# Optimization experiments

Hardware: AMD Instinct MI355X
Metric: run time of the kernel (lower is better)

The kernel has to match this reference:

```python
import jax, jax.numpy as jnp
import numpy as np

# ---- static config (matches init_kwargs) ----
NLAT, NLON = 181, 360
LMAX = NLAT                 # hard_thresholding_fraction = 1.0
MMAX = NLON // 2 + 1        # 181, real FFT in longitude
INC = 26
OUTC = 26
EMBED = 256
NLAYERS = 4
MLP_HID = int(EMBED * 2.0)
EPS = 1e-6


def _legendre(lmax, mmax, theta):
    """Orthonormal associated Legendre functions Pbar[l, m, k] at colatitudes theta."""
    ct, st = np.cos(theta), np.sin(theta)
    K = theta.size
    P = np.zeros((lmax, mmax, K), dtype=np.float64)
    P[0, 0] = np.sqrt(1.0 / (4.0 * np.pi))
    for m in range(1, mmax):
        P[m, m] = -np.sqrt((2.0 * m + 1.0) / (2.0 * m)) * st * P[m - 1, m - 1]
    for m in range(mmax):
        if m + 1 < lmax:
            P[m + 1, m] = np.sqrt(2.0 * m + 3.0) * ct * P[m, m]
        for l in range(m + 2, lmax):
            a = np.sqrt((4.0 * l * l - 1.0) / (l * l - m * m))
            b = np.sqrt(((2.0 * l + 1.0) * (l - 1.0 + m) * (l - 1.0 - m)) / ((2.0 * l - 3.0) * (l * l - m * m)))
            P[l, m] = a * ct * P[l - 1, m] - b * P[l - 2, m]
    return P

# equiangular grid + quadrature weights; precompute analysis/synthesis matrices
_theta = np.linspace(0.0, np.pi, NLAT)
_wq = (np.pi / (NLAT - 1)) * np.sin(_theta)
_P = _legendre(LMAX, MMAX, _theta)
PW = jnp.asarray((_P * (2.0 * np.pi * _wq)[None, None, :]).astype(np.float32))  # analysis
PS = jnp.asarray(_P.astype(np.float32))                                         # synthesis


def _ln(x):
    # per-pixel layer norm over channel dim, no affine (affine_norms=False)
    mu = jnp.mean(x, axis=1, keepdims=True)
    var = jnp.mean((x - mu) ** 2, axis=1, keepdims=True)
    return (x - mu) * jax.lax.rsqrt(var + EPS)


def _conv1x1(x, w, b=None):
    y = jnp.einsum('oi,bihw->bohw', w, x)
    return y if b is None else y + b[None, :, None, None]


def _sht(x):
    # x: (b,c,nlat,nlon) -> coeff (b,c,l,m) complex64
    F = jnp.fft.rfft(x, axis=-1) / NLON          # (b,c,k,m)
    return jnp.einsum('lmk,bckm->bclm', PW, F)


def _isht(c):
    F = jnp.einsum('lmk,bclm->bckm', PS, c)      # (b,c,k,m)
    return jnp.fft.irfft(F * NLON, n=NLON, axis=-1)


def _block(x, wsp, bsp, wis, bis, wf1, bf1, wf2, bf2):
    xn = _ln(x)                                  # norm0
    c = _sht(xn)
    co = jnp.einsum('oil,bilm->bolm', wsp, c)    # dhconv: diagonal in m, dense per l
    y = _isht(co) + bsp[None, :, None, None]
    x1 = y + _conv1x1(xn, wis, bis)              # inner linear skip (residual = filter input)
    x1 = jax.nn.gelu(x1, approximate=False)
    x2 = _ln(x1)                                 # norm1
    h = jax.nn.gelu(_conv1x1(x2, wf1, bf1), approximate=False)
    x2 = _conv1x1(h, wf2, bf2)                   # MLP
    return x2 + xn                               # outer identity skip


def setup_inputs() -> dict:
    key = jax.random.key(0)
    ks = jax.random.split(key, 10)
    n = jax.random.normal
    x = n(ks[0], (1, INC, NLAT, NLON), jnp.float32)
    w_enc = n(ks[1], (EMBED, INC), jnp.float32) * float(1.0 / np.sqrt(INC))
    b_enc = jnp.zeros((EMBED,), jnp.float32)
    pos_emb = n(ks[2], (1, EMBED, NLAT, NLON), jnp.float32) * 0.02
    w_spec = n(ks[3], (NLAYERS, EMBED, EMBED, LMAX), jnp.float32) * float(1.0 / np.sqrt(EMBED))
    b_spec = jnp.zeros((NLAYERS, EMBED), jnp.float32)
    w_iskip = n(ks[4], (NLAYERS, EMBED, EMBED), jnp.float32) * float(1.0 / np.sqrt(EMBED))
    b_iskip = jnp.zeros((NLAYERS, EMBED), jnp.float32)
    w_fc1 = n(ks[5], (NLAYERS, MLP_HID, EMBED), jnp.float32) * float(1.0 / np.sqrt(EMBED))
    b_fc1 = jnp.zeros((NLAYERS, MLP_HID), jnp.float32)
    w_fc2 = n(ks[6], (NLAYERS, EMBED, MLP_HID), jnp.float32) * float(1.0 / np.sqrt(MLP_HID))
    b_fc2 = jnp.zeros((NLAYERS, EMBED), jnp.float32)
    w_dec = n(ks[7], (OUTC, EMBED + INC), jnp.float32) * float(1.0 / np.sqrt(EMBED + INC))
    b_dec = jnp.zeros((OUTC,), jnp.float32)
    return {'x': x, 'w_enc': w_enc, 'b_enc': b_enc, 'pos_emb': pos_emb,
            'w_spec': w_spec, 'b_spec': b_spec, 'w_iskip': w_iskip, 'b_iskip': b_iskip,
            'w_fc1': w_fc1, 'b_fc1': b_fc1, 'w_fc2': w_fc2, 'b_fc2': b_fc2,
            'w_dec': w_dec, 'b_dec': b_dec}


def reference(x, w_enc, b_enc, pos_emb, w_spec, b_spec, w_iskip, b_iskip,
              w_fc1, b_fc1, w_fc2, b_fc2, w_dec, b_dec):
    res = x                                       # big_skip residual (raw input)
    h = _conv1x1(x, w_enc, b_enc) + pos_emb       # encoder + pos embed
    for i in range(NLAYERS):
        h = _block(h, w_spec[i], b_spec[i], w_iskip[i], b_iskip[i],
                   w_fc1[i], b_fc1[i], w_fc2[i], b_fc2[i])
    h = jnp.concatenate([h, res], axis=1)         # big skip concat
    return _conv1x1(h, w_dec, b_dec)
```

## Files before the change

### kernel.cpp

```cpp
#include <hip/hip_runtime.h>
#include <math.h>

#define NLATg 181
#define NLONg 360
#define PIXg  65160
#define EMBg  256
#define MHIDg 512
#define PLANEg 8386816
#define PKSTR 184
#define PMSTR2 33304

#define FLAG_GELU 1
#define FLAG_ACC  2
#define FLAG_F32  4
#define FLAG_BF16 8

typedef unsigned short u16;
typedef unsigned int   u32;
typedef __attribute__((ext_vector_type(8))) short bf16x8;
typedef __attribute__((ext_vector_type(4))) float f32x4;

__device__ __forceinline__ float gelu_f(float x) {
    return 0.5f * x * (1.0f + erff(x * 0.70710678118654752440f));
}

__device__ __forceinline__ void split_f(float v, u16& h, u16& l) {
    u32 u = __float_as_uint(v);
    h = (u16)(u >> 16);
    float hf = __uint_as_float(u & 0xFFFF0000u);
    l = (u16)(__float_as_uint(v - hf) >> 16);
}

__device__ __forceinline__ void glds16(const u16* g, u16* l) {
    __builtin_amdgcn_global_load_lds((const __attribute__((address_space(1))) u32*)g,
                                     (__attribute__((address_space(3))) u32*)l, 16, 0, 0);
}


__global__ __launch_bounds__(256) void init_legendre(u16* __restrict__ Pah, u16* __restrict__ Pal,
                                                     u16* __restrict__ Psh, u16* __restrict__ Psl) {
    int idx = blockIdx.x * 256 + threadIdx.x;
    if (idx >= 181 * 181) return;
    int m = idx / 181, k = idx % 181;
    if (k < 3) {
        for (int l = 0; l < 181; ++l) {
            size_t o = (size_t)m * PMSTR2 + (size_t)l * PKSTR + 181 + k;
            Pah[o] = 0; Pal[o] = 0;
        }
    }
    for (int j = 181; j < PKSTR; ++j) {
        size_t o = (size_t)m * PMSTR2 + (size_t)k * PKSTR + j;
        Psh[o] = 0; Psl[o] = 0;
    }
    double theta = M_PI * (double)k / 180.0;
    double ct = cos(theta), st = sin(theta);
    double pmm = sqrt(1.0 / (4.0 * M_PI));
    for (int j = 1; j <= m; ++j) pmm *= -sqrt((2.0 * j + 1.0) / (2.0 * j)) * st;
    u16 h, lo;
    auto emit = [&](int l, double v) {
        split_f((float)v, h, lo);
        size_t oa = (size_t)m * PMSTR2 + (size_t)l * PKSTR + k;
        size_t os = (size_t)m * PMSTR2 + (size_t)k * PKSTR + l;
        Pah[oa] = h; Pal[oa] = lo;
        Psh[os] = h; Psl[os] = lo;
    };
    for (int l2 = 0; l2 < m; ++l2) emit(l2, 0.0);
    emit(m, pmm);
    if (m + 1 < 181) {
        double pl1 = sqrt(2.0 * m + 3.0) * ct * pmm;
        emit(m + 1, pl1);
        double pl2 = pmm;
        for (int ll = m + 2; ll < 181; ++ll) {
            double L = ll, M2 = m;
            double a = sqrt((4.0 * L * L - 1.0) / (L * L - M2 * M2));
            double b = sqrt(((2.0 * L + 1.0) * (L - 1.0 + M2) * (L - 1.0 - M2)) /
                            ((2.0 * L - 3.0) * (L * L - M2 * M2)));
            double p = a * ct * pl1 - b * pl2;
            emit(ll, p);
            pl2 = pl1; pl1 = p;
        }
    }
}

__global__ __launch_bounds__(256) void init_trig(u16* __restrict__ Eh, u16* __restrict__ El,
                                                 u16* __restrict__ DtTh, u16* __restrict__ DtTl,
                                                 float* __restrict__ wqs, u16* __restrict__ zpb) {
    int idx = blockIdx.x * 256 + threadIdx.x;
    if (idx < 8) zpb[idx] = 0;
    if (idx < 181) {
        double theta = M_PI * (double)idx / 180.0;
        wqs[idx] = (float)(2.0 * M_PI * (M_PI / 180.0) * sin(theta) / 360.0);
    }
    if (idx >= 181 * 360) return;
    int m = idx / 360, n = idx % 360;
    int a = (m * n) % 360;
    double ang = M_PI * (double)a / 180.0;
    double c = cos(ang), s = sin(ang);
    u16 h, l;
    split_f((float)c, h, l);        Eh[idx] = h;        El[idx] = l;
    split_f((float)(-s), h, l);     Eh[PIXg + idx] = h; El[PIXg + idx] = l;
    double cm = (m == 0 || m == 180) ? 1.0 : 2.0;
    split_f((float)(cm * c), h, l);
    DtTh[(size_t)n * 384 + m] = h;        DtTl[(size_t)n * 384 + m] = l;
    split_f((float)(-cm * s), h, l);
    DtTh[(size_t)n * 384 + 181 + m] = h;  DtTl[(size_t)n * 384 + 181 + m] = l;
    if (m == 0) {
        for (int j = 362; j < 384; ++j) { DtTh[(size_t)n * 384 + j] = 0; DtTl[(size_t)n * 384 + j] = 0; }
    }
}

__global__ __launch_bounds__(256) void transpose_wspec(const float* __restrict__ W,
                                                       u16* __restrict__ WTh, u16* __restrict__ WTl) {
    __shared__ float tile[32][33];
    int l0 = blockIdx.x * 32, o0 = blockIdx.y * 32, i = blockIdx.z;
    int c = threadIdx.x & 31, r = threadIdx.x >> 5;
#pragma unroll
    for (int j = 0; j < 4; j++) {
        int row = r + j * 8;
        float v = 0.f;
        if (l0 + c < 181) v = W[(size_t)(o0 + row) * 46336 + i * 181 + (l0 + c)];
        tile[row][c] = v;
    }
    __syncthreads();
#pragma unroll
    for (int j = 0; j < 4; j++) {
        int row = r + j * 8;
        if (l0 + row < 181) {
            u16 h, l; split_f(tile[c][row], h, l);
            size_t o = (size_t)(l0 + row) * 65536 + i * 256 + (o0 + c);
            WTh[o] = h; WTl[o] = l;
        }
    }
}

__global__ __launch_bounds__(256) void split_bf16(const float* __restrict__ in,
                                                  u16* __restrict__ h, u16* __restrict__ l, int n) {
    int i = blockIdx.x * 256 + threadIdx.x;
    if (i >= n) return;
    u16 hh, ll; split_f(in[i], hh, ll);
    h[i] = hh; l[i] = ll;
}

__global__ __launch_bounds__(256) void ln_kernel(const float* __restrict__ X, float* __restrict__ Y,
                                                 u16* __restrict__ YTh, u16* __restrict__ YTl) {
    int p0 = blockIdx.x * 64;
    int t = threadIdx.x;
    int ps = t & 63, cg = t >> 6;
    int p = p0 + ps;
    bool ok = p < PIXg;
    float sum = 0.f, sumsq = 0.f;
    if (ok) {
        for (int c = cg; c < EMBg; c += 4) {
            float v = X[(size_t)c * PIXg + p];
            sum += v; sumsq += v * v;
        }
    }
    __shared__ float s1[4][64];
    __shared__ float s2[4][64];
    s1[cg][ps] = sum; s2[cg][ps] = sumsq;
    __syncthreads();
    float tot  = s1[0][ps] + s1[1][ps] + s1[2][ps] + s1[3][ps];
    float tot2 = s2[0][ps] + s2[1][ps] + s2[2][ps] + s2[3][ps];
    float mu = tot * (1.0f / 256.0f);
    float var = tot2 * (1.0f / 256.0f) - mu * mu;
    float inv = rsqrtf(var + 1e-6f);
    if (ok) {
        for (int c = cg; c < EMBg; c += 4) {
            size_t offp = (size_t)c * PIXg + p;
            float v = (X[offp] - mu) * inv;
            if (Y) Y[offp] = v;
            u16 h, l; split_f(v, h, l);
            size_t ot = (size_t)p * 256 + c;
            YTh[ot] = h; YTl[ot] = l;
        }
    }
}

__global__ __launch_bounds__(256) void gelu_bias(float* __restrict__ X, const float* __restrict__ b) {
    int idx = blockIdx.x * 256 + threadIdx.x;
    int c = idx / 16290;
    float bv = b[c];
    float4 v = reinterpret_cast<float4*>(X)[idx];
    v.x = gelu_f(v.x + bv); v.y = gelu_f(v.y + bv);
    v.z = gelu_f(v.z + bv); v.w = gelu_f(v.w + bv);
    reinterpret_cast<float4*>(X)[idx] = v;
}

__global__ __launch_bounds__(256, 2) void gemm_f32(
    const float* __restrict__ A, int Ars, int Acs, int Azs, int Aps,
    const float* __restrict__ B, int Brs, int Bcs, int Bzs, int Bps,
    float* __restrict__ C, int Crs, int Ccs, int Czs, int Cps,
    const float* __restrict__ bias, const float* __restrict__ zscale,
    const float* __restrict__ resid,
    int M, int N, int K, int Zin, int flags)
{
    int z = blockIdx.z;
    if (z >= Zin) { z -= Zin; A += Aps; B += Bps; C += Cps; if (resid) resid += Cps; }
    A += (size_t)z * Azs; B += (size_t)z * Bzs; C += (size_t)z * Czs;
    if (resid) resid += (size_t)z * Czs;

    const int bm = blockIdx.y * 128, bn = blockIdx.x * 128;
    const int t = threadIdx.x;
    const int tx = t & 15, ty = t >> 4;

    __shared__ float As[16][132];
    __shared__ float Bs[16][132];

    float acc[8][8];
#pragma unroll
    for (int i = 0; i < 8; i++)
#pragma unroll
        for (int j = 0; j < 8; j++) acc[i][j] = 0.0f;

    for (int k0 = 0; k0 < K; k0 += 16) {
        if (Acs == 1) {
            int kk = t & 15, r = t >> 4;
            int gk = k0 + kk; bool kv = gk < K;
#pragma unroll
            for (int i = 0; i < 8; i++) {
                int gr = bm + r + i * 16; if (gr > M - 1) gr = M - 1;
                As[kk][r + i * 16] = kv ? A[(size_t)gr * Ars + gk] : 0.f;
            }
        } else {
            int row = t & 127, kb = t >> 7;
            int gr = bm + row; if (gr > M - 1) gr = M - 1;
            size_t base = (size_t)gr * Ars;
#pragma unroll
            for (int i = 0; i < 8; i++) {
                int gk = k0 + kb + i * 2;
                As[kb + i * 2][row] = (gk < K) ? A[base + (size_t)gk * Acs] : 0.f;
            }
        }
        if (Bcs == 1) {
            int col = t & 127, kb = t >> 7;
            int gc = bn + col; if (gc > N - 1) gc = N - 1;
#pragma unroll
            for (int i = 0; i < 8; i++) {
                int gk = k0 + kb + i * 2;
                Bs[kb + i * 2][col] = (gk < K) ? B[(size_t)gk * Brs + gc] : 0.f;
            }
        } else {
            int kk = t & 15, cb = t >> 4;
            int gk = k0 + kk; bool kv = gk < K;
#pragma unroll
            for (int i = 0; i < 8; i++) {
                int gc = bn + cb + i * 16; if (gc > N - 1) gc = N - 1;
                Bs[kk][cb + i * 16] = kv ? B[(size_t)gk * Brs + (size_t)gc * Bcs] : 0.f;
            }
        }
        __syncthreads();
#pragma unroll
        for (int kk = 0; kk < 16; kk++) {
            float4 a0 = *(const float4*)&As[kk][ty * 4];
            float4 a1 = *(const float4*)&As[kk][ty * 4 + 64];
            float4 b0 = *(const float4*)&Bs[kk][tx * 4];
            float4 b1 = *(const float4*)&Bs[kk][tx * 4 + 64];
            float av[8] = {a0.x, a0.y, a0.z, a0.w, a1.x, a1.y, a1.z, a1.w};
            float bv[8] = {b0.x, b0.y, b0.z, b0.w, b1.x, b1.y, b1.z, b1.w};
#pragma unroll
            for (int i = 0; i < 8; i++)
#pragma unroll
                for (int j = 0; j < 8; j++)
                    acc[i][j] = fmaf(av[i], bv[j], acc[i][j]);
        }
        __syncthreads();
    }

    const float zs = zscale ? zscale[z] : 1.0f;
    const bool fastN = (Ccs == 1) && (bn + 128 <= N);
#pragma unroll
    for (int i = 0; i < 8; i++) {
        int gi = bm + ty * 4 + (i & 3) + ((i >> 2) << 6);
        if (gi >= M) continue;
        float bval = bias ? bias[gi] : 0.0f;
        size_t crow = (size_t)gi * (size_t)Crs;
        if (fastN) {
#pragma unroll
            for (int h = 0; h < 2; h++) {
                int gj = bn + tx * 4 + h * 64;
                size_t off = crow + (size_t)gj;
                float4 v;
                v.x = acc[i][h * 4 + 0] * zs + bval;
                v.y = acc[i][h * 4 + 1] * zs + bval;
                v.z = acc[i][h * 4 + 2] * zs + bval;
                v.w = acc[i][h * 4 + 3] * zs + bval;
                if (resid) { float4 r = *(const float4*)&resid[off];
                             v.x += r.x; v.y += r.y; v.z += r.z; v.w += r.w; }
                if (flags & FLAG_GELU) { v.x = gelu_f(v.x); v.y = gelu_f(v.y);
                                         v.z = gelu_f(v.z); v.w = gelu_f(v.w); }
                if (flags & FLAG_ACC)  { float4 c0 = *(const float4*)&C[off];
                                         v.x += c0.x; v.y += c0.y; v.z += c0.z; v.w += c0.w; }
                *(float4*)&C[off] = v;
            }
        } else {
#pragma unroll
            for (int j = 0; j < 8; j++) {
                int gj = bn + tx * 4 + (j & 3) + ((j >> 2) << 6);
                if (gj >= N) continue;
                size_t off = crow + (size_t)gj * (size_t)Ccs;
                float v = acc[i][j] * zs + bval;
                if (resid) v += resid[off];
                if (flags & FLAG_GELU) v = gelu_f(v);
                if (flags & FLAG_ACC) v += C[off];
                C[off] = v;
            }
        }
    }
}

__global__ __launch_bounds__(256, 1) void gemm_bf16(
    const u16* __restrict__ Ah, const u16* __restrict__ Al,
    int Ars, int Acs, int Azs, int Aps,
    const u16* __restrict__ Bh, const u16* __restrict__ Bl,
    int Brs, int Bcs, int Bzs, int Bps,
    float* __restrict__ C, u16* __restrict__ Ch, u16* __restrict__ Cl,
    int Crs, int Ccs, int Czs, int Cps,
    const float* __restrict__ bias, const float* __restrict__ biasN,
    const float* __restrict__ zscale, const float* __restrict__ resid,
    const u16* __restrict__ zp,
    int M, int N, int K, int Zin, int flags)
{
    int z = blockIdx.z;
    if (z >= Zin) {
        z -= Zin;
        Ah += Aps; Al += Aps; Bh += Bps; Bl += Bps;
        if (C) C += Cps;
        if (Ch) Ch += Cps;
        if (Cl) Cl += Cps;
        if (resid) resid += Cps;
    }
    Ah += (size_t)z * Azs; Al += (size_t)z * Azs;
    Bh += (size_t)z * Bzs; Bl += (size_t)z * Bzs;
    const size_t czoff = (size_t)z * Czs;

    const int t = threadIdx.x;
    const int lane = t & 63;
    const int w = t >> 6;
    const int bm = blockIdx.y * 128, bn = blockIdx.x * 128;

    __shared__ u16 Ahs[128 * 40];
    __shared__ u16 Als[128 * 40];
    __shared__ u16 Bhs[128 * 40];
    __shared__ u16 Bls[128 * 40];

    f32x4 acc[4][4];
#pragma unroll
    for (int i = 0; i < 4; i++)
#pragma unroll
        for (int j = 0; j < 4; j++) acc[i][j] = (f32x4){0.f, 0.f, 0.f, 0.f};

    const int wm = (w >> 1) * 64, wn = (w & 1) * 64;
    const int fr = lane & 15, fgb = lane >> 4;
    const bool ag = (Acs == 1), bg = (Brs == 1);
    const int K8 = (K + 7) & ~7;
    const int rloc = lane >> 2, csl = lane & 3;

    int aoff[4], boff[4];
#pragma unroll
    for (int f = 0; f < 4; f++) {
        int ra = wm + f * 16 + fr;
        aoff[f] = ag ? (ra * 32 + ((fgb ^ ((ra >> 1) & 3)) << 3))
                     : (ra * 40 + (((fgb ^ (ra >> 3)) & 3) << 3));
        int rb = wn + f * 16 + fr;
        boff[f] = bg ? (rb * 32 + ((fgb ^ ((rb >> 1) & 3)) << 3))
                     : (rb * 40 + (((fgb ^ (rb >> 3)) & 3) << 3));
    }

    for (int k0 = 0; k0 < K; k0 += 32) {
        if (ag) {
#pragma unroll
            for (int inst = 0; inst < 2; ++inst) {
                int r = w * 32 + inst * 16 + rloc;
                int gr = bm + r; if (gr > M - 1) gr = M - 1;
                int gk = k0 + 8 * (csl ^ ((r >> 1) & 3));
                const u16* sh = zp; const u16* sl = zp;
                if (gk < K8) { size_t o = (size_t)gr * Ars + gk; sh = Ah + o; sl = Al + o; }
                glds16(sh, &Ahs[(w * 32 + inst * 16) * 32]);
                glds16(sl, &Als[(w * 32 + inst * 16) * 32]);
            }
        } else {
            int ml = (t & 63) * 2;
            int kg = t >> 6;
            int gr0 = bm + ml;     if (gr0 > M - 1) gr0 = M - 1;
            int gr1 = bm + ml + 1; if (gr1 > M - 1) gr1 = M - 1;
            bool pair = (gr1 == gr0 + 1);
            u32 vah[8], val8[8];
#pragma unroll
            for (int i = 0; i < 8; i++) {
                int kk = kg + 4 * i;
                int gk = k0 + kk;
                u32 vh = 0, vl = 0;
                if (gk < K) {
                    size_t o = (size_t)gk * Acs + gr0;
                    if (pair) { vh = *(const u32*)(Ah + o); vl = *(const u32*)(Al + o); }
                    else {
                        vh = Ah[o]; vl = Al[o];
                        u32 h1 = Ah[(size_t)gk * Acs + gr1], l1 = Al[(size_t)gk * Acs + gr1];
                        vh |= h1 << 16; vl |= l1 << 16;
                    }
                }
                vah[i] = vh; val8[i] = vl;
            }
#pragma unroll
            for (int i = 0; i < 8; i++) {
                int kk = kg + 4 * i;
                int blk = (kk >> 3) & 3;
                int s0 = ml * 40 + (((blk ^ (ml >> 3)) & 3) << 3) + (kk & 7);
                int s1 = (ml + 1) * 40 + (((blk ^ ((ml + 1) >> 3)) & 3) << 3) + (kk & 7);
                Ahs[s0] = (u16)vah[i]; Ahs[s1] = (u16)(vah[i] >> 16);
                Als[s0] = (u16)val8[i]; Als[s1] = (u16)(val8[i] >> 16);
            }
        }
        if (bg) {
#pragma unroll
            for (int inst = 0; inst < 2; ++inst) {
                int cidx = w * 32 + inst * 16 + rloc;
                int gj = bn + cidx; if (gj > N - 1) gj = N - 1;
                int gk = k0 + 8 * (csl ^ ((cidx >> 1) & 3));
                const u16* sh = zp; const u16* sl = zp;
                if (gk < K8) { size_t o = (size_t)gj * Bcs + gk; sh = Bh + o; sl = Bl + o; }
                glds16(sh, &Bhs[(w * 32 + inst * 16) * 32]);
                glds16(sl, &Bls[(w * 32 + inst * 16) * 32]);
            }
        } else {
            int jl = (t & 63) * 2;
            int kg = t >> 6;
            int gj0 = bn + jl;     if (gj0 > N - 1) gj0 = N - 1;
            int gj1 = bn + jl + 1; if (gj1 > N - 1) gj1 = N - 1;
            bool pair = (gj1 == gj0 + 1);
            u32 vbh[8], vbl[8];
#pragma unroll
            for (int i = 0; i < 8; i++) {
                int kk = kg + 4 * i;
                int gk = k0 + kk;
                u32 vh = 0, vl = 0;
                if (gk < K) {
                    size_t o = (size_t)gk * Brs + gj0;
                    if (pair) { vh = *(const u32*)(Bh + o); vl = *(const u32*)(Bl + o); }
                    else {
                        vh = Bh[o]; vl = Bl[o];
                        u32 h1 = Bh[(size_t)gk * Brs + gj1], l1 = Bl[(size_t)gk * Brs + gj1];
                        vh |= h1 << 16; vl |= l1 << 16;
                    }
                }
                vbh[i] = vh; vbl[i] = vl;
            }
#pragma unroll
            for (int i = 0; i < 8; i++) {
                int kk = kg + 4 * i;
                int blk = (kk >> 3) & 3;
                int s0 = jl * 40 + (((blk ^ (jl >> 3)) & 3) << 3) + (kk & 7);
                int s1 = (jl + 1) * 40 + (((blk ^ ((jl + 1) >> 3)) & 3) << 3) + (kk & 7);
                Bhs[s0] = (u16)vbh[i]; Bhs[s1] = (u16)(vbh[i] >> 16);
                Bls[s0] = (u16)vbl[i]; Bls[s1] = (u16)(vbl[i] >> 16);
            }
        }
        __syncthreads();

        {
            bf16x8 fah[4], fbh[4];
#pragma unroll
            for (int f = 0; f < 4; f++) {
                fah[f] = *(const bf16x8*)(Ahs + aoff[f]);
                fbh[f] = *(const bf16x8*)(Bhs + boff[f]);
            }
#pragma unroll
            for (int i = 0; i < 4; i++)
#pragma unroll
                for (int j = 0; j < 4; j++)
                    acc[i][j] = __builtin_amdgcn_mfma_f32_16x16x32_bf16(fah[i], fbh[j], acc[i][j], 0, 0, 0);
            bf16x8 fbl[4];
#pragma unroll
            for (int f = 0; f < 4; f++) fbl[f] = *(const bf16x8*)(Bls + boff[f]);
#pragma unroll
            for (int i = 0; i < 4; i++)
#pragma unroll
                for (int j = 0; j < 4; j++)
                    acc[i][j] = __builtin_amdgcn_mfma_f32_16x16x32_bf16(fah[i], fbl[j], acc[i][j], 0, 0, 0);
            bf16x8 fal[4];
#pragma unroll
            for (int f = 0; f < 4; f++) fal[f] = *(const bf16x8*)(Als + aoff[f]);
#pragma unroll
            for (int i = 0; i < 4; i++)
#pragma unroll
                for (int j = 0; j < 4; j++)
                    acc[i][j] = __builtin_amdgcn_mfma_f32_16x16x32_bf16(fal[i], fbh[j], acc[i][j], 0, 0, 0);
        }
        __syncthreads();
    }

    const float zs = zscale ? zscale[z] : 1.0f;
#pragma unroll
    for (int i = 0; i < 4; i++) {
#pragma unroll
        for (int r = 0; r < 4; r++) {
            int grow = bm + wm + i * 16 + (lane >> 4) * 4 + r;
            if (grow >= M) continue;
            float bval = bias ? bias[grow] : 0.0f;
            size_t rowoff = czoff + (size_t)grow * Crs;
#pragma unroll
            for (int j = 0; j < 4; j++) {
                int gcol = bn + wn + j * 16 + fr;
                if (gcol >= N) continue;
                size_t off = rowoff + (size_t)gcol * Ccs;
                float v = acc[i][j][r] * zs + bval;
                if (biasN) v += biasN[gcol];
                if (resid) v += resid[off];
                if (flags & FLAG_ACC) v += C[off];
                if (flags & FLAG_GELU) v = gelu_f(v);
                if (flags & FLAG_F32) C[off] = v;
                if (flags & FLAG_BF16) {
                    u16 h, l; split_f(v, h, l);
                    Ch[off] = h; Cl[off] = l;
                }
            }
        }
    }
}

static inline void launch_gemm(hipStream_t s,
    const float* A, int Ars, int Acs, int Azs, int Aps,
    const float* B, int Brs, int Bcs, int Bzs, int Bps,
    float* C, int Crs, int Ccs, int Czs, int Cps,
    const float* bias, const float* zscale, const float* resid,
    int M, int N, int K, int Zin, int nplanes, int flags)
{
    dim3 grid((N + 127) / 128, (M + 127) / 128, Zin * nplanes);
    hipLaunchKernelGGL(gemm_f32, grid, dim3(256), 0, s,
                       A, Ars, Acs, Azs, Aps, B, Brs, Bcs, Bzs, Bps,
                       C, Crs, Ccs, Czs, Cps, bias, zscale, resid,
                       M, N, K, Zin, flags);
}

static inline void launch_gemm16(hipStream_t s,
    const u16* Ah, const u16* Al, int Ars, int Acs, int Azs, int Aps,
    const u16* Bh, const u16* Bl, int Brs, int Bcs, int Bzs, int Bps,
    float* C, u16* Ch, u16* Cl, int Crs, int Ccs, int Czs, int Cps,
    const float* bias, const float* biasN, const float* zscale, const float* resid,
    const u16* zp, int M, int N, int K, int Zin, int nplanes, int flags)
{
    dim3 grid((N + 127) / 128, (M + 127) / 128, Zin * nplanes);
    hipLaunchKernelGGL(gemm_bf16, grid, dim3(256), 0, s,
                       Ah, Al, Ars, Acs, Azs, Aps, Bh, Bl, Brs, Bcs, Bzs, Bps,
                       C, Ch, Cl, Crs, Ccs, Czs, Cps, bias, biasN, zscale, resid, zp,
                       M, N, K, Zin, flags);
}

extern "C" void kernel_launch(void* const* d_in, const int* in_sizes, int n_in,
                              void* d_out, int out_size, void* d_ws, size_t ws_size,
                              hipStream_t stream)
{
    const float* x      = (const float*)d_in[0];
    const float* w_enc  = (const float*)d_in[1];
    const float* b_enc  = (const float*)d_in[2];
    const float* pos    = (const float*)d_in[3];
    const float* w_spec = (const float*)d_in[4];
    const float* b_spec = (const float*)d_in[5];
    const float* w_is   = (const float*)d_in[6];
    const float* b_is   = (const float*)d_in[7];
    const float* w_f1   = (const float*)d_in[8];
    const float* b_f1   = (const float*)d_in[9];
    const float* w_f2   = (const float*)d_in[10];
    const float* b_f2   = (const float*)d_in[11];
    const float* w_dec  = (const float*)d_in[12];
    const float* b_dec  = (const float*)d_in[13];
    float* out = (float*)d_out;

    char* base = (char*)d_ws;
    size_t off = 0;
    auto alloc = [&](size_t bytes) { size_t o = off; off += (bytes + 255) & ~(size_t)255; return o; };
    u16* Pah = (u16*)(base + alloc(12056048));
    u16* Pal = (u16*)(base + alloc(12056048));
    u16* Psh = (u16*)(base + alloc(12056048));
    u16* Psl = (u16*)(base + alloc(12056048));
    u16* Eh  = (u16*)(base + alloc(260640));
    u16* El  = (u16*)(base + alloc(260640));
    u16* DtTh = (u16*)(base + alloc(276480));
    u16* DtTl = (u16*)(base + alloc(276480));
    float* wqs = (float*)(base + alloc(724));
    u16* zp  = (u16*)(base + alloc(256));
    u16* SP  = (u16*)(base + alloc(134189056));
    u16* S0h = SP;
    u16* S0l = SP + 16773632;
    u16* S1h = SP + 2 * 16773632;
    u16* S1l = SP + 3 * 16773632;
    u16* hmlpTh = SP;
    u16* hmlpTl = SP + 33361920;
    float* xn  = (float*)(base + alloc(66723840));
    u16* xnTh = (u16*)(base + alloc(33361920));
    u16* xnTl = (u16*)(base + alloc(33361920));
    float* hbuf = (float*)(base + alloc(66723840));
    float* tA   = (float*)(base + alloc(66723840));
    u16* wth = (u16*)tA;
    u16* wtl = wth + 11862016;
    u16* wish = (u16*)(base + alloc(131072));
    u16* wisl = (u16*)(base + alloc(131072));
    u16* wf1h = (u16*)(base + alloc(262144));
    u16* wf1l = (u16*)(base + alloc(262144));
    u16* wf2h = (u16*)(base + alloc(262144));
    u16* wf2l = (u16*)(base + alloc(262144));

    init_legendre<<<(181 * 181 + 255) / 256, 256, 0, stream>>>(Pah, Pal, Psh, Psl);
    init_trig<<<(181 * 360 + 255) / 256, 256, 0, stream>>>(Eh, El, DtTh, DtTl, wqs, zp);

    launch_gemm(stream, w_enc, 26, 1, 0, 0,  x, PIXg, 1, 0, 0,  hbuf, PIXg, 1, 0, 0,
                b_enc, nullptr, pos, EMBg, PIXg, 26, 1, 1, 0);

    for (int L = 0; L < 4; ++L) {
        const float* wsp = w_spec + (size_t)L * EMBg * EMBg * 181;
        const float* bsp = b_spec + (size_t)L * EMBg;
        const float* wis = w_is   + (size_t)L * EMBg * EMBg;
        const float* bis = b_is   + (size_t)L * EMBg;
        const float* wf1 = w_f1   + (size_t)L * MHIDg * EMBg;
        const float* bf1 = b_f1   + (size_t)L * MHIDg;
        const float* wf2 = w_f2   + (size_t)L * EMBg * MHIDg;
        const float* bf2 = b_f2   + (size_t)L * EMBg;

        transpose_wspec<<<dim3(6, 8, 256), 256, 0, stream>>>(wsp, wth, wtl);
        split_bf16<<<(65536 + 255) / 256, 256, 0, stream>>>(wis, wish, wisl, 65536);
        split_bf16<<<(131072 + 255) / 256, 256, 0, stream>>>(wf1, wf1h, wf1l, 131072);
        split_bf16<<<(131072 + 255) / 256, 256, 0, stream>>>(wf2, wf2h, wf2l, 131072);

        ln_kernel<<<1019, 256, 0, stream>>>(hbuf, xn, xnTh, xnTl);

        launch_gemm16(stream, Eh, El, 360, 1, 0, PIXg,  xnTh, xnTl, 256, 1, 92160, 0,
                      nullptr, S0h, S0l, 46336, 1, 256, PLANEg,
                      nullptr, nullptr, wqs, nullptr, zp, 181, 256, 360, 181, 2, FLAG_BF16);
        launch_gemm16(stream, Pah, Pal, PKSTR, 1, PMSTR2, 0,  S0h, S0l, 256, 1, 46336, PLANEg,
                      nullptr, S1h, S1l, 46336, 1, 256, PLANEg,
                      nullptr, nullptr, nullptr, nullptr, zp, 181, 256, 181, 181, 2, FLAG_BF16);
        launch_gemm16(stream, S1h, S1l, 256, 1, 46336, PLANEg,  wth, wtl, 256, 1, 65536, 0,
                      nullptr, S0h, S0l, 46336, 1, 256, PLANEg,
                      nullptr, nullptr, nullptr, nullptr, zp, 181, 256, 256, 181, 2, FLAG_BF16);
        launch_gemm16(stream, Psh, Psl, PKSTR, 1, PMSTR2, 0,  S0h, S0l, 256, 1, 46336, PLANEg,
                      nullptr, S1h, S1l, 92672, 1, 256, 46336,
                      nullptr, nullptr, nullptr, nullptr, zp, 181, 256, 181, 181, 2, FLAG_BF16);
        launch_gemm16(stream, S1h, S1l, 1, 256, 92672, 0,  DtTh, DtTl, 1, 384, 0, 0,
                      tA, nullptr, nullptr, PIXg, 1, 360, 0,
                      nullptr, nullptr, nullptr, nullptr, zp, 256, 360, 362, 181, 1, FLAG_F32);
        launch_gemm16(stream, wish, wisl, 256, 1, 0, 0,  xnTh, xnTl, 1, 256, 0, 0,
                      tA, nullptr, nullptr, PIXg, 1, 0, 0,
                      bis, nullptr, nullptr, nullptr, zp, 256, PIXg, 256, 1, 1, FLAG_F32 | FLAG_ACC);
        gelu_bias<<<16290, 256, 0, stream>>>(tA, bsp);
        ln_kernel<<<1019, 256, 0, stream>>>(tA, nullptr, xnTh, xnTl);
        launch_gemm16(stream, xnTh, xnTl, 256, 1, 0, 0,  wf1h, wf1l, 1, 256, 0, 0,
                      nullptr, hmlpTh, hmlpTl, 512, 1, 0, 0,
                      nullptr, bf1, nullptr, nullptr, zp, PIXg, 512, 256, 1, 1, FLAG_BF16 | FLAG_GELU);
        launch_gemm16(stream, wf2h, wf2l, 512, 1, 0, 0,  hmlpTh, hmlpTl, 1, 512, 0, 0,
                      hbuf, nullptr, nullptr, PIXg, 1, 0, 0,
                      bf2, nullptr, nullptr, xn, zp, EMBg, PIXg, 512, 1, 1, FLAG_F32);
    }

    launch_gemm(stream, w_dec, 282, 1, 0, 0,  hbuf, PIXg, 1, 0, 0,  out, PIXg, 1, 0, 0,
                b_dec, nullptr, nullptr, 26, PIXg, 256, 1, 1, 0);
    launch_gemm(stream, w_dec + 256, 282, 1, 0, 0,  x, PIXg, 1, 0, 0,  out, PIXg, 1, 0, 0,
                nullptr, nullptr, nullptr, 26, PIXg, 26, 1, 1, FLAG_ACC);
}
```

Measured before the change: 8.685 ms.

## Double-buffer LDS tiles in bf16 GEMM and remap workgroups across XCDs

The split-bf16 GEMM now keeps two LDS buffers per operand. It stages the next K-slice while the MFMAs run on the current one, which removes one barrier per iteration and overlaps global loads with compute. It also remaps the linear workgroup id so that consecutive tiles land on the same XCD, which is meant to improve L2 locality. The cost is doubled LDS use per block and extra index arithmetic, and the non-async register-staged path may lengthen register live ranges.

```diff
diff --git a/kernel.cpp b/kernel.cpp
--- a/kernel.cpp
+++ b/kernel.cpp
@@ -9,6 +9,7 @@
 #define PLANEg 8386816
 #define PKSTR 184
 #define PMSTR2 33304
+#define LBUF 5120
 
 #define FLAG_GELU 1
 #define FLAG_ACC  2
@@ -320,7 +321,19 @@
     const u16* __restrict__ zp,
     int M, int N, int K, int Zin, int flags)
 {
-    int z = blockIdx.z;
+    unsigned gx = gridDim.x, gy = gridDim.y;
+    unsigned nwg = gx * gy * gridDim.z;
+    unsigned hw = (blockIdx.z * gy + blockIdx.y) * gx + blockIdx.x;
+    unsigned wid2 = hw;
+    if (nwg >= 16) {
+        unsigned q = nwg >> 3, r2 = nwg & 7;
+        unsigned xcd = hw & 7, sl = hw >> 3;
+        wid2 = (xcd < r2 ? xcd * (q + 1) : r2 * (q + 1) + (xcd - r2) * q) + sl;
+    }
+    unsigned bxu = wid2 % gx; unsigned t2 = wid2 / gx;
+    unsigned byu = t2 % gy;   unsigned bzu = t2 / gy;
+
+    int z = (int)bzu;
     if (z >= Zin) {
         z -= Zin;
         Ah += Aps; Al += Aps; Bh += Bps; Bl += Bps;
@@ -336,12 +349,12 @@
     const int t = threadIdx.x;
     const int lane = t & 63;
     const int w = t >> 6;
-    const int bm = blockIdx.y * 128, bn = blockIdx.x * 128;
-
-    __shared__ u16 Ahs[128 * 40];
-    __shared__ u16 Als[128 * 40];
-    __shared__ u16 Bhs[128 * 40];
-    __shared__ u16 Bls[128 * 40];
+    const int bm = (int)byu * 128, bn = (int)bxu * 128;
+
+    __shared__ u16 Ahs[2 * LBUF];
+    __shared__ u16 Als[2 * LBUF];
+    __shared__ u16 Bhs[2 * LBUF];
+    __shared__ u16 Bls[2 * LBUF];
 
     f32x4 acc[4][4];
 #pragma unroll
@@ -366,7 +379,7 @@
                      : (rb * 40 + (((fgb ^ (rb >> 3)) & 3) << 3));
     }
 
-    for (int k0 = 0; k0 < K; k0 += 32) {
+    auto stage = [&](int bo, int k0) {
         if (ag) {
 #pragma unroll
             for (int inst = 0; inst < 2; ++inst) {
@@ -375,8 +388,8 @@
                 int gk = k0 + 8 * (csl ^ ((r >> 1) & 3));
                 const u16* sh = zp; const u16* sl = zp;
                 if (gk < K8) { size_t o = (size_t)gr * Ars + gk; sh = Ah + o; sl = Al + o; }
-                glds16(sh, &Ahs[(w * 32 + inst * 16) * 32]);
-                glds16(sl, &Als[(w * 32 + inst * 16) * 32]);
+                glds16(sh, &Ahs[bo + (w * 32 + inst * 16) * 32]);
+                glds16(sl, &Als[bo + (w * 32 + inst * 16) * 32]);
             }
         } else {
             int ml = (t & 63) * 2;
@@ -405,8 +418,8 @@
             for (int i = 0; i < 8; i++) {
                 int kk = kg + 4 * i;
                 int blk = (kk >> 3) & 3;
-                int s0 = ml * 40 + (((blk ^ (ml >> 3)) & 3) << 3) + (kk & 7);
-                int s1 = (ml + 1) * 40 + (((blk ^ ((ml + 1) >> 3)) & 3) << 3) + (kk & 7);
+                int s0 = bo + ml * 40 + (((blk ^ (ml >> 3)) & 3) << 3) + (kk & 7);
+                int s1 = bo + (ml + 1) * 40 + (((blk ^ ((ml + 1) >> 3)) & 3) << 3) + (kk & 7);
                 Ahs[s0] = (u16)vah[i]; Ahs[s1] = (u16)(vah[i] >> 16);
                 Als[s0] = (u16)val8[i]; Als[s1] = (u16)(val8[i] >> 16);
             }
@@ -419,8 +432,8 @@
                 int gk = k0 + 8 * (csl ^ ((cidx >> 1) & 3));
                 const u16* sh = zp; const u16* sl = zp;
                 if (gk < K8) { size_t o = (size_t)gj * Bcs + gk; sh = Bh + o; sl = Bl + o; }
-                glds16(sh, &Bhs[(w * 32 + inst * 16) * 32]);
-                glds16(sl, &Bls[(w * 32 + inst * 16) * 32]);
+                glds16(sh, &Bhs[bo + (w * 32 + inst * 16) * 32]);
+                glds16(sl, &Bls[bo + (w * 32 + inst * 16) * 32]);
             }
         } else {
             int jl = (t & 63) * 2;
@@ -449,20 +462,29 @@
             for (int i = 0; i < 8; i++) {
                 int kk = kg + 4 * i;
                 int blk = (kk >> 3) & 3;
-                int s0 = jl * 40 + (((blk ^ (jl >> 3)) & 3) << 3) + (kk & 7);
-                int s1 = (jl + 1) * 40 + (((blk ^ ((jl + 1) >> 3)) & 3) << 3) + (kk & 7);
+                int s0 = bo + jl * 40 + (((blk ^ (jl >> 3)) & 3) << 3) + (kk & 7);
+                int s1 = bo + (jl + 1) * 40 + (((blk ^ ((jl + 1) >> 3)) & 3) << 3) + (kk & 7);
                 Bhs[s0] = (u16)vbh[i]; Bhs[s1] = (u16)(vbh[i] >> 16);
                 Bls[s0] = (u16)vbl[i]; Bls[s1] = (u16)(vbl[i] >> 16);
             }
         }
-        __syncthreads();
-
+    };
+
+    stage(0, 0);
+    __syncthreads();
+
+    int cur = 0;
+    for (int k0 = 0; k0 < K; k0 += 32) {
+        int nb = cur ^ 1;
+        if (k0 + 32 < K) stage(nb * LBUF, k0 + 32);
+
+        const int co = cur * LBUF;
         {
             bf16x8 fah[4], fbh[4];
 #pragma unroll
             for (int f = 0; f < 4; f++) {
-                fah[f] = *(const bf16x8*)(Ahs + aoff[f]);
-                fbh[f] = *(const bf16x8*)(Bhs + boff[f]);
+                fah[f] = *(const bf16x8*)(Ahs + co + aoff[f]);
+                fbh[f] = *(const bf16x8*)(Bhs + co + boff[f]);
             }
 #pragma unroll
             for (int i = 0; i < 4; i++)
@@ -471,7 +493,7 @@
                     acc[i][j] = __builtin_amdgcn_mfma_f32_16x16x32_bf16(fah[i], fbh[j], acc[i][j], 0, 0, 0);
             bf16x8 fbl[4];
 #pragma unroll
-            for (int f = 0; f < 4; f++) fbl[f] = *(const bf16x8*)(Bls + boff[f]);
+            for (int f = 0; f < 4; f++) fbl[f] = *(const bf16x8*)(Bls + co + boff[f]);
 #pragma unroll
             for (int i = 0; i < 4; i++)
 #pragma unroll
@@ -479,7 +501,7 @@
                     acc[i][j] = __builtin_amdgcn_mfma_f32_16x16x32_bf16(fah[i], fbl[j], acc[i][j], 0, 0, 0);
             bf16x8 fal[4];
 #pragma unroll
-            for (int f = 0; f < 4; f++) fal[f] = *(const bf16x8*)(Als + aoff[f]);
+            for (int f = 0; f < 4; f++) fal[f] = *(const bf16x8*)(Als + co + aoff[f]);
 #pragma unroll
             for (int i = 0; i < 4; i++)
 #pragma unroll
@@ -487,6 +509,7 @@
                     acc[i][j] = __builtin_amdgcn_mfma_f32_16x16x32_bf16(fal[i], fbh[j], acc[i][j], 0, 0, 0);
         }
         __syncthreads();
+        cur = nb;
     }
 
     const float zs = zscale ? zscale[z] : 1.0f;
```

New measurement: 8.614 ms. About the same (-0.8%).
